# Optimization experiments

Measured on AMD Instinct MI355X. Metric: run time of the kernel, lower is better.

Reference implementation:

```python
import jax, jax.numpy as jnp
import numpy as np

N_HEADS = 8
D_EMBED = 512
D_HEAD = D_EMBED // N_HEADS


def setup_inputs() -> dict:
    key = jax.random.key(0)
    ks = jax.random.split(key, 5)
    s = 1.0 / np.sqrt(D_EMBED)
    return {
        "x": jax.random.normal(ks[0], (2, 4096, D_EMBED), dtype=jnp.float32),
        "in_proj_w": jax.random.normal(ks[1], (3 * D_EMBED, D_EMBED), dtype=jnp.float32) * s,
        "in_proj_b": jax.random.normal(ks[2], (3 * D_EMBED,), dtype=jnp.float32) * s,
        "out_proj_w": jax.random.normal(ks[3], (D_EMBED, D_EMBED), dtype=jnp.float32) * s,
        "out_proj_b": jax.random.normal(ks[4], (D_EMBED,), dtype=jnp.float32) * s,
    }


def reference(x, in_proj_w, in_proj_b, out_proj_w, out_proj_b):
    B, S, D = x.shape
    # in_proj: x @ W^T + b, then chunk into q, k, v
    qkv = jnp.einsum("bsd,ed->bse", x, in_proj_w) + in_proj_b  # [B,S,3D]
    q, k, v = jnp.split(qkv, 3, axis=-1)
    # [B,S,D] -> [B,H,S,dh]
    def heads(t):
        return t.reshape(B, S, N_HEADS, D_HEAD).transpose(0, 2, 1, 3)
    q, k, v = heads(q), heads(k), heads(v)
    scale = 1.0 / np.sqrt(D_HEAD).astype(np.float32)
    scores = jnp.einsum("bhqd,bhkd->bhqk", q, k) * scale  # [B,H,S,S]
    attn = jax.nn.softmax(scores, axis=-1)
    out = jnp.einsum("bhqk,bhkd->bhqd", attn, v)  # [B,H,S,dh]
    out = out.transpose(0, 2, 1, 3).reshape(B, S, D)
    return jnp.einsum("bsd,ed->bse", out, out_proj_w) + out_proj_b
```

## Files before the change

kernel.cpp:

```cpp
#include <hip/hip_runtime.h>
#include <cstdint>
#include <cstddef>

typedef __bf16 bf16x8 __attribute__((ext_vector_type(8)));
typedef float f32x4 __attribute__((ext_vector_type(4)));
typedef float f32x16 __attribute__((ext_vector_type(16)));
typedef unsigned int u32x4 __attribute__((ext_vector_type(4)));
typedef unsigned short u16;
typedef unsigned short u16x8 __attribute__((ext_vector_type(8)));
typedef unsigned int u32;

#define S_LEN 4096
#define NH 8
#define DH 64
#define D_EMB 512
#define BATCH 2
#define M_ROWS 8192
#define GK 512
#define QSCALE 0.18033688011112042f

__device__ __forceinline__ u16 f2bf(float f) {
  u32 u = __builtin_bit_cast(u32, f);
  u += 0x7FFFu + ((u >> 16) & 1u);
  return (u16)(u >> 16);
}
__device__ __forceinline__ float bf2f(u16 v) {
  return __builtin_bit_cast(float, (u32)v << 16);
}
__device__ __forceinline__ u32 pk2(float a, float b) {
  union { __bf16 h[2]; u32 w; } u;
  u.h[0] = (__bf16)a;
  u.h[1] = (__bf16)b;
  return u.w;
}
__device__ __forceinline__ float fexp2(float x) {
#if __has_builtin(__builtin_amdgcn_exp2f)
  return __builtin_amdgcn_exp2f(x);
#else
  return __expf(x * 0.6931471805599453f);
#endif
}

#define MFMA32(a, b, c) __builtin_amdgcn_mfma_f32_32x32x16_bf16(a, b, c, 0, 0, 0)

#define GLD_LDS16(gsrc, ldst)                                                        \
  __builtin_amdgcn_global_load_lds(                                                  \
      (const __attribute__((address_space(1))) void*)(gsrc),                         \
      (__attribute__((address_space(3))) void*)(ldst), 16, 0, 0)

__global__ void detect_kernel(const u16* __restrict__ x, int* __restrict__ flag) {
  __shared__ int cnt;
  if (threadIdx.x == 0) cnt = 0;
  __syncthreads();
  int plaus = 0;
  for (int i = threadIdx.x; i < 2048; i += 256) {
    u16 u = x[2 * i];
    int ex = (u >> 7) & 0xFF;
    plaus += (ex >= 100 && ex <= 134) ? 1 : 0;
  }
  atomicAdd(&cnt, plaus);
  __syncthreads();
  if (threadIdx.x == 0) *flag = (cnt > 1024) ? 0 : 1;
}

__global__ void prep_kernel(const void* __restrict__ x, const void* __restrict__ wq,
                            const void* __restrict__ bq, const void* __restrict__ wo,
                            const void* __restrict__ bo,
                            u16* __restrict__ xb, u16* __restrict__ wqb,
                            u16* __restrict__ wob, float* __restrict__ bqf,
                            float* __restrict__ bof, const int* __restrict__ flag) {
  const bool f32 = (*flag != 0);
  const size_t i = (size_t)blockIdx.x * blockDim.x + threadIdx.x;
  if (i < (size_t)M_ROWS * D_EMB)
    xb[i] = f32 ? f2bf(((const float*)x)[i]) : ((const u16*)x)[i];
  if (i < (size_t)3 * D_EMB * D_EMB)
    wqb[i] = f32 ? f2bf(((const float*)wq)[i]) : ((const u16*)wq)[i];
  if (i < (size_t)D_EMB * D_EMB)
    wob[i] = f32 ? f2bf(((const float*)wo)[i]) : ((const u16*)wo)[i];
  if (i < 3 * D_EMB)
    bqf[i] = f32 ? ((const float*)bq)[i] : bf2f(((const u16*)bq)[i]);
  if (i < D_EMB)
    bof[i] = f32 ? ((const float*)bo)[i] : bf2f(((const u16*)bo)[i]);
}

template <int EPI>
__global__ __launch_bounds__(256, 2)
void gemm_bt(const u16* __restrict__ A, const u16* __restrict__ B, int N,
             const float* __restrict__ bias, u16* __restrict__ qout,
             u16* __restrict__ kout, u16* __restrict__ vout, u16* __restrict__ obf,
             float* __restrict__ of32, const int* __restrict__ flag) {
  __shared__ u16 As[128 * 64];
  __shared__ u16 Bs[128 * 64];
  const int tid = threadIdx.x;
  const int wave = tid >> 6, lane = tid & 63;
  const int m0 = blockIdx.x * 128;
  const int n0 = blockIdx.y * 128;
  const int wr = (wave >> 1) * 64, wc = (wave & 1) * 64;

  const int sr = wave * 8 + (lane >> 3);
  const int scb = (lane & 7) * 16;

  f32x4 acc[4][4] = {};

  for (int k0 = 0; k0 < GK; k0 += 64) {
#pragma unroll
    for (int i = 0; i < 4; ++i) {
      const int r = i * 32 + sr;
      const int sc = (scb ^ ((r & 7) << 4)) >> 1;
      GLD_LDS16(A + (size_t)(m0 + r) * GK + k0 + sc, As + i * 2048 + wave * 512);
    }
#pragma unroll
    for (int i = 0; i < 4; ++i) {
      const int r = i * 32 + sr;
      const int sc = (scb ^ ((r & 7) << 4)) >> 1;
      GLD_LDS16(B + (size_t)(n0 + r) * GK + k0 + sc, Bs + i * 2048 + wave * 512);
    }
    __syncthreads();
#pragma unroll
    for (int kk = 0; kk < 2; ++kk) {
      const int cb = kk * 64 + ((lane >> 4) << 4);
      bf16x8 a[4], b[4];
#pragma unroll
      for (int m = 0; m < 4; ++m) {
        const int r = wr + m * 16 + (lane & 15);
        a[m] = *(const bf16x8*)((const char*)As + r * 128 + (cb ^ ((r & 7) << 4)));
      }
#pragma unroll
      for (int n = 0; n < 4; ++n) {
        const int r = wc + n * 16 + (lane & 15);
        b[n] = *(const bf16x8*)((const char*)Bs + r * 128 + (cb ^ ((r & 7) << 4)));
      }
#pragma unroll
      for (int m = 0; m < 4; ++m)
#pragma unroll
        for (int n = 0; n < 4; ++n)
          acc[m][n] = __builtin_amdgcn_mfma_f32_16x16x32_bf16(a[m], b[n], acc[m][n], 0, 0, 0);
    }
    __syncthreads();
  }

  const bool f32out = (EPI == 1) && (*flag != 0);
#pragma unroll
  for (int n = 0; n < 4; ++n) {
    const int col = n0 + wc + n * 16 + (lane & 15);
    const float bv = bias[col];
#pragma unroll
    for (int m = 0; m < 4; ++m) {
#pragma unroll
      for (int r = 0; r < 4; ++r) {
        const int row = m0 + wr + m * 16 + ((lane >> 4) << 2) + r;
        float v = acc[m][n][r] + bv;
        if (EPI == 0) {
          const int bb = row >> 12, s = row & 4095;
          const int which = col >> 9, hc = col & 511;
          const int h = hc >> 6, d = hc & 63;
          const int bh = bb * NH + h;
          if (which == 2) {
            const int t16 = s >> 4, dblk = d >> 5;
            const int lane_ = ((s >> 3) & 1) * 32 + (d & 31);
            const int j = s & 7;
            vout[(((size_t)(bh * 256 + t16) * 2 + dblk) * 64 + lane_) * 8 + j] = f2bf(v);
          } else {
            const int t32 = s >> 5, dk = d >> 4;
            const int lane_ = ((d >> 3) & 1) * 32 + (s & 31);
            const int j = d & 7;
            u16* dst = (which == 0) ? qout : kout;
            const float vv = (which == 0) ? v * QSCALE : v;
            dst[(((size_t)(bh * 128 + t32) * 4 + dk) * 64 + lane_) * 8 + j] = f2bf(vv);
          }
        } else {
          if (f32out)
            of32[(size_t)row * D_EMB + col] = v;
          else
            obf[(size_t)row * D_EMB + col] = f2bf(v);
        }
      }
    }
  }
}

__global__ __launch_bounds__(256, 4)
void flash_attn(const u16* __restrict__ qfrag, const u16* __restrict__ kfrag,
                const u16* __restrict__ vfrag, u16* __restrict__ op0,
                u16* __restrict__ op1, float* __restrict__ ml) {
  const int phys = blockIdx.x;
  const int xcd = phys & 7, slot = phys >> 3;
  const int bh = xcd * 2 + (slot >> 6);
  const int rem = slot & 63;
  const int qb = rem >> 1;
  const int hf = rem & 1;

  const int lane = threadIdx.x & 63;
  const int wave = threadIdx.x >> 6;
  const int l31 = lane & 31, hi = lane >> 5;
  const int q0 = qb * 128 + wave * 32;

  bf16x8 qf[4];
  {
    const u16* qb_ = qfrag + ((size_t)(bh * 128 + (q0 >> 5)) * 4) * 512 + lane * 8;
#pragma unroll
    for (int dk = 0; dk < 4; ++dk) qf[dk] = *(const bf16x8*)(qb_ + dk * 512);
  }

  const u16* kb_ = kfrag + (size_t)bh * (128 * 4 * 512) + lane * 8;
  const u16* vb_ = vfrag + (size_t)bh * (256 * 2 * 512) + lane * 8;

  f32x16 accO0 = {}, accO1 = {};
  float m = -1e30f, lst = 0.f;

  const int kvbeg = hf * (S_LEN / 2);
  const int kvend = kvbeg + (S_LEN / 2);

#pragma unroll 1
  for (int kv0 = kvbeg; kv0 < kvend; kv0 += 32) {
    const int t32 = kv0 >> 5, t16 = kv0 >> 4;
    bf16x8 kf[4], vfA[2], vfB[2];
#pragma unroll
    for (int dk = 0; dk < 4; ++dk)
      kf[dk] = *(const bf16x8*)(kb_ + (size_t)(t32 * 4 + dk) * 512);
    vfA[0] = *(const bf16x8*)(vb_ + (size_t)((t16 + 0) * 2 + 0) * 512);
    vfB[0] = *(const bf16x8*)(vb_ + (size_t)((t16 + 0) * 2 + 1) * 512);
    vfA[1] = *(const bf16x8*)(vb_ + (size_t)((t16 + 1) * 2 + 0) * 512);
    vfB[1] = *(const bf16x8*)(vb_ + (size_t)((t16 + 1) * 2 + 1) * 512);

    f32x16 s = {};
#pragma unroll
    for (int dk = 0; dk < 4; ++dk) s = MFMA32(kf[dk], qf[dk], s);

    float mx8[8];
#pragma unroll
    for (int i = 0; i < 8; ++i) mx8[i] = fmaxf(s[i], s[i + 8]);
    float mx4[4];
#pragma unroll
    for (int i = 0; i < 4; ++i) mx4[i] = fmaxf(mx8[i], mx8[i + 4]);
    const float mown = fmaxf(fmaxf(mx4[0], mx4[1]), fmaxf(mx4[2], mx4[3]));
    const float pf = fmaxf(mown, __shfl_xor(mown, 32, 64));

    if (!__all(pf - m <= 8.0f)) {
      const float mn = fmaxf(m, pf);
      const float alpha = fexp2(m - mn);
      m = mn;
      lst *= alpha;
#pragma unroll
      for (int r = 0; r < 16; ++r) {
        const int qrow = (r & 3) + 8 * (r >> 2) + 4 * hi;
        const float ar = __shfl(alpha, qrow, 64);
        accO0[r] *= ar;
        accO1[r] *= ar;
      }
    }

#pragma unroll
    for (int i = 0; i < 16; ++i) s[i] = fexp2(s[i] - m);
    float sm8[8];
#pragma unroll
    for (int i = 0; i < 8; ++i) sm8[i] = s[i] + s[i + 8];
    float sm4[4];
#pragma unroll
    for (int i = 0; i < 4; ++i) sm4[i] = sm8[i] + sm8[i + 4];
    const float sown = (sm4[0] + sm4[1]) + (sm4[2] + sm4[3]);
    lst += sown + __shfl_xor(sown, 32, 64);

    u32 W0, W1, W2, W3;
#define PACK8(P, B0)                                                   \
    {                                                                  \
      const u32 w0 = pk2(P[B0 + 0], P[B0 + 1]);                        \
      const u32 w1 = pk2(P[B0 + 2], P[B0 + 3]);                        \
      const u32 w2 = pk2(P[B0 + 4], P[B0 + 5]);                        \
      const u32 w3 = pk2(P[B0 + 6], P[B0 + 7]);                        \
      const u32 rA = (u32)__shfl_xor((int)(hi ? w0 : w2), 32, 64);     \
      const u32 rB = (u32)__shfl_xor((int)(hi ? w1 : w3), 32, 64);     \
      W0 = hi ? rA : w0;                                               \
      W1 = hi ? rB : w1;                                               \
      W2 = hi ? w2 : rA;                                               \
      W3 = hi ? w3 : rB;                                               \
    }

    bf16x8 pa;
    PACK8(s, 0);
    pa = __builtin_bit_cast(bf16x8, (u32x4){W0, W1, W2, W3});
    accO0 = MFMA32(pa, vfA[0], accO0);
    accO1 = MFMA32(pa, vfB[0], accO1);
    PACK8(s, 8);
    pa = __builtin_bit_cast(bf16x8, (u32x4){W0, W1, W2, W3});
    accO0 = MFMA32(pa, vfA[1], accO0);
    accO1 = MFMA32(pa, vfB[1], accO1);
#undef PACK8
  }

  u16* op = hf ? op1 : op0;
#pragma unroll
  for (int r = 0; r < 16; ++r) {
    const int qrow = (r & 3) + 8 * (r >> 2) + 4 * hi;
    const size_t R = (size_t)bh * S_LEN + q0 + qrow;
    op[R * 64 + l31] = f2bf(accO0[r]);
    op[R * 64 + 32 + l31] = f2bf(accO1[r]);
  }
  if (hi == 0) {
    const size_t R = (size_t)bh * S_LEN + q0 + l31;
    ml[((size_t)hf * 65536 + R) * 2 + 0] = m;
    ml[((size_t)hf * 65536 + R) * 2 + 1] = lst;
  }
}

__global__ __launch_bounds__(256)
void merge_kernel(const u16* __restrict__ op0, const u16* __restrict__ op1,
                  const float* __restrict__ ml, u16* __restrict__ ao) {
  const int idx = blockIdx.x * 256 + threadIdx.x;
  const int R = idx >> 3;
  const int dd = (idx & 7) * 8;
  const float m0 = ml[(size_t)R * 2 + 0], l0 = ml[(size_t)R * 2 + 1];
  const float m1 = ml[((size_t)65536 + R) * 2 + 0], l1 = ml[((size_t)65536 + R) * 2 + 1];
  const float M = fmaxf(m0, m1);
  float w0 = fexp2(m0 - M), w1 = fexp2(m1 - M);
  const float rL = 1.f / (l0 * w0 + l1 * w1);
  w0 *= rL;
  w1 *= rL;
  const u16x8 a = *(const u16x8*)(op0 + (size_t)R * 64 + dd);
  const u16x8 c = *(const u16x8*)(op1 + (size_t)R * 64 + dd);
  u16x8 o;
#pragma unroll
  for (int j = 0; j < 8; ++j) o[j] = f2bf(bf2f(a[j]) * w0 + bf2f(c[j]) * w1);
  const int bh = R >> 12, s = R & 4095;
  const int b = bh >> 3, h = bh & 7;
  *(u16x8*)(ao + ((size_t)(b * S_LEN + s) * D_EMB + h * DH + dd)) = o;
}

extern "C" void kernel_launch(void* const* d_in, const int* in_sizes, int n_in,
                              void* d_out, int out_size, void* d_ws, size_t ws_size,
                              hipStream_t stream) {
  char* w = (char*)d_ws;
  int* flag = (int*)w;
  u16* xb = (u16*)(w + 256);
  u16* wqb = (u16*)(w + 8388864);
  u16* wob = (u16*)(w + 9961728);
  float* bqf = (float*)(w + 10486016);
  float* bof = (float*)(w + 10492160);
  u16* qfr = (u16*)(w + 10494208);
  u16* kfr = (u16*)(w + 18882816);
  u16* vfr = (u16*)(w + 27271424);
  u16* ao = (u16*)(w + 35660032);
  u16* op1 = (u16*)(w + 44048640);
  u16* op0 = xb;
  float* ml = (float*)wqb;

  detect_kernel<<<1, 256, 0, stream>>>((const u16*)d_in[0], flag);
  prep_kernel<<<16384, 256, 0, stream>>>(d_in[0], d_in[1], d_in[2], d_in[3], d_in[4],
                                         xb, wqb, wob, bqf, bof, flag);
  gemm_bt<0><<<dim3(64, 12), 256, 0, stream>>>(xb, wqb, 3 * D_EMB, bqf, qfr, kfr, vfr,
                                               nullptr, nullptr, flag);
  flash_attn<<<1024, 256, 0, stream>>>(qfr, kfr, vfr, op0, op1, ml);
  merge_kernel<<<2048, 256, 0, stream>>>(op0, op1, ml, ao);
  gemm_bt<1><<<dim3(64, 4), 256, 0, stream>>>(ao, wob, D_EMB, bof, nullptr, nullptr,
                                              nullptr, (u16*)d_out, (float*)d_out, flag);
}
```

Before: 160.4 us.

## Split KV across waves in-block and merge partials in LDS, dropping merge kernel

Each flash-attention block now owns 32 query rows. Its four waves each process a quarter of the KV sequence, and the partial outputs are combined in shared memory using per-row max/sum rescaling. The final bf16 output is written directly in the [B,S,D] layout, so the separate merge kernel and the global round-trip of partial outputs and m/l statistics go away. The grid doubles, launch bounds now ask for 8 blocks per CU, and the serialized LDS accumulation adds several barriers per block.

New measurement: 552.1 us. 3.44x slower.

```diff
diff --git a/kernel.cpp b/kernel.cpp
--- a/kernel.cpp
+++ b/kernel.cpp
@@ -179,49 +179,50 @@
   }
 }
 
-__global__ __launch_bounds__(256, 4)
+__global__ __launch_bounds__(256, 8)
 void flash_attn(const u16* __restrict__ qfrag, const u16* __restrict__ kfrag,
-                const u16* __restrict__ vfrag, u16* __restrict__ op0,
-                u16* __restrict__ op1, float* __restrict__ ml) {
+                const u16* __restrict__ vfrag, u16* __restrict__ ao) {
+  __shared__ float Ols[32][65];
+  __shared__ float Mls[4][32][2];
+
   const int phys = blockIdx.x;
   const int xcd = phys & 7, slot = phys >> 3;
-  const int bh = xcd * 2 + (slot >> 6);
-  const int rem = slot & 63;
-  const int qb = rem >> 1;
-  const int hf = rem & 1;
+  const int bh = xcd * 2 + (slot >> 7);
+  const int qi = slot & 127;
+  const int b = bh >> 3, h = bh & 7;
+  const int q0 = qi * 32;
 
   const int lane = threadIdx.x & 63;
-  const int wave = threadIdx.x >> 6;
+  const int hf = threadIdx.x >> 6;
   const int l31 = lane & 31, hi = lane >> 5;
-  const int q0 = qb * 128 + wave * 32;
 
   bf16x8 qf[4];
   {
-    const u16* qb_ = qfrag + ((size_t)(bh * 128 + (q0 >> 5)) * 4) * 512 + lane * 8;
+    const u16* qb_ = qfrag + ((size_t)(bh * 128 + qi) * 4) * 512 + lane * 8;
 #pragma unroll
     for (int dk = 0; dk < 4; ++dk) qf[dk] = *(const bf16x8*)(qb_ + dk * 512);
   }
 
-  const u16* kb_ = kfrag + (size_t)bh * (128 * 4 * 512) + lane * 8;
-  const u16* vb_ = vfrag + (size_t)bh * (256 * 2 * 512) + lane * 8;
+  const u16* kptr = kfrag + (size_t)bh * (128 * 4 * 512) +
+                    (size_t)(hf * 32) * 4 * 512 + lane * 8;
+  const u16* vptr = vfrag + (size_t)bh * (256 * 2 * 512) +
+                    (size_t)(hf * 64) * 2 * 512 + lane * 8;
 
   f32x16 accO0 = {}, accO1 = {};
   float m = -1e30f, lst = 0.f;
 
-  const int kvbeg = hf * (S_LEN / 2);
-  const int kvend = kvbeg + (S_LEN / 2);
-
 #pragma unroll 1
-  for (int kv0 = kvbeg; kv0 < kvend; kv0 += 32) {
-    const int t32 = kv0 >> 5, t16 = kv0 >> 4;
+  for (int it = 0; it < 32; ++it) {
     bf16x8 kf[4], vfA[2], vfB[2];
 #pragma unroll
     for (int dk = 0; dk < 4; ++dk)
-      kf[dk] = *(const bf16x8*)(kb_ + (size_t)(t32 * 4 + dk) * 512);
-    vfA[0] = *(const bf16x8*)(vb_ + (size_t)((t16 + 0) * 2 + 0) * 512);
-    vfB[0] = *(const bf16x8*)(vb_ + (size_t)((t16 + 0) * 2 + 1) * 512);
-    vfA[1] = *(const bf16x8*)(vb_ + (size_t)((t16 + 1) * 2 + 0) * 512);
-    vfB[1] = *(const bf16x8*)(vb_ + (size_t)((t16 + 1) * 2 + 1) * 512);
+      kf[dk] = *(const bf16x8*)(kptr + dk * 512);
+    vfA[0] = *(const bf16x8*)(vptr);
+    vfB[0] = *(const bf16x8*)(vptr + 512);
+    vfA[1] = *(const bf16x8*)(vptr + 1024);
+    vfB[1] = *(const bf16x8*)(vptr + 1536);
+    kptr += 2048;
+    vptr += 2048;
 
     f32x16 s = {};
 #pragma unroll
@@ -288,42 +289,49 @@
 #undef PACK8
   }
 
-  u16* op = hf ? op1 : op0;
-#pragma unroll
-  for (int r = 0; r < 16; ++r) {
-    const int qrow = (r & 3) + 8 * (r >> 2) + 4 * hi;
-    const size_t R = (size_t)bh * S_LEN + q0 + qrow;
-    op[R * 64 + l31] = f2bf(accO0[r]);
-    op[R * 64 + 32 + l31] = f2bf(accO1[r]);
-  }
   if (hi == 0) {
-    const size_t R = (size_t)bh * S_LEN + q0 + l31;
-    ml[((size_t)hf * 65536 + R) * 2 + 0] = m;
-    ml[((size_t)hf * 65536 + R) * 2 + 1] = lst;
-  }
-}
-
-__global__ __launch_bounds__(256)
-void merge_kernel(const u16* __restrict__ op0, const u16* __restrict__ op1,
-                  const float* __restrict__ ml, u16* __restrict__ ao) {
-  const int idx = blockIdx.x * 256 + threadIdx.x;
-  const int R = idx >> 3;
-  const int dd = (idx & 7) * 8;
-  const float m0 = ml[(size_t)R * 2 + 0], l0 = ml[(size_t)R * 2 + 1];
-  const float m1 = ml[((size_t)65536 + R) * 2 + 0], l1 = ml[((size_t)65536 + R) * 2 + 1];
-  const float M = fmaxf(m0, m1);
-  float w0 = fexp2(m0 - M), w1 = fexp2(m1 - M);
-  const float rL = 1.f / (l0 * w0 + l1 * w1);
-  w0 *= rL;
-  w1 *= rL;
-  const u16x8 a = *(const u16x8*)(op0 + (size_t)R * 64 + dd);
-  const u16x8 c = *(const u16x8*)(op1 + (size_t)R * 64 + dd);
-  u16x8 o;
-#pragma unroll
-  for (int j = 0; j < 8; ++j) o[j] = f2bf(bf2f(a[j]) * w0 + bf2f(c[j]) * w1);
-  const int bh = R >> 12, s = R & 4095;
-  const int b = bh >> 3, h = bh & 7;
-  *(u16x8*)(ao + ((size_t)(b * S_LEN + s) * D_EMB + h * DH + dd)) = o;
+    Mls[hf][l31][0] = m;
+    Mls[hf][l31][1] = lst;
+  }
+  __syncthreads();
+  float M = -1e30f;
+#pragma unroll
+  for (int i = 0; i < 4; ++i) M = fmaxf(M, Mls[i][l31][0]);
+  float L = 0.f;
+#pragma unroll
+  for (int i = 0; i < 4; ++i) L += Mls[i][l31][1] * fexp2(Mls[i][l31][0] - M);
+  const float w = fexp2(m - M) / L;
+
+#define DEPOSIT(OP)                                                    \
+  {                                                                    \
+    _Pragma("unroll")                                                  \
+    for (int r = 0; r < 16; ++r) {                                     \
+      const int qrow = (r & 3) + 8 * (r >> 2) + 4 * hi;                \
+      const float wr_ = __shfl(w, qrow, 64);                           \
+      Ols[qrow][l31] OP accO0[r] * wr_;                                \
+      Ols[qrow][32 + l31] OP accO1[r] * wr_;                           \
+    }                                                                  \
+  }
+
+  if (hf == 0) DEPOSIT(=);
+  __syncthreads();
+  if (hf == 1) DEPOSIT(+=);
+  __syncthreads();
+  if (hf == 2) DEPOSIT(+=);
+  __syncthreads();
+  if (hf == 3) {
+#pragma unroll
+    for (int r = 0; r < 16; ++r) {
+      const int qrow = (r & 3) + 8 * (r >> 2) + 4 * hi;
+      const float wr_ = __shfl(w, qrow, 64);
+      const float o0 = accO0[r] * wr_ + Ols[qrow][l31];
+      const float o1 = accO1[r] * wr_ + Ols[qrow][32 + l31];
+      u16* orow = ao + (size_t)(b * S_LEN + q0 + qrow) * D_EMB + h * DH;
+      orow[l31] = f2bf(o0);
+      orow[32 + l31] = f2bf(o1);
+    }
+  }
+#undef DEPOSIT
 }
 
 extern "C" void kernel_launch(void* const* d_in, const int* in_sizes, int n_in,
@@ -340,17 +348,13 @@
   u16* kfr = (u16*)(w + 18882816);
   u16* vfr = (u16*)(w + 27271424);
   u16* ao = (u16*)(w + 35660032);
-  u16* op1 = (u16*)(w + 44048640);
-  u16* op0 = xb;
-  float* ml = (float*)wqb;
 
   detect_kernel<<<1, 256, 0, stream>>>((const u16*)d_in[0], flag);
   prep_kernel<<<16384, 256, 0, stream>>>(d_in[0], d_in[1], d_in[2], d_in[3], d_in[4],
                                          xb, wqb, wob, bqf, bof, flag);
   gemm_bt<0><<<dim3(64, 12), 256, 0, stream>>>(xb, wqb, 3 * D_EMB, bqf, qfr, kfr, vfr,
                                                nullptr, nullptr, flag);
-  flash_attn<<<1024, 256, 0, stream>>>(qfr, kfr, vfr, op0, op1, ml);
-  merge_kernel<<<2048, 256, 0, stream>>>(op0, op1, ml, ao);
+  flash_attn<<<2048, 256, 0, stream>>>(qfr, kfr, vfr, ao);
   gemm_bt<1><<<dim3(64, 4), 256, 0, stream>>>(ao, wob, D_EMB, bof, nullptr, nullptr,
                                               nullptr, (u16*)d_out, (float*)d_out, flag);
 }
```
